# Optimization experiments

Measured on AMD Instinct MI355X. Metric: run time of the kernel, lower is better.

The kernel has to match this reference:

```python
import jax, jax.numpy as jnp
import numpy as np

B, N, L, D_MODEL, H, D_K, D_V = 8, 307, 64, 64, 4, 16, 16


def setup_inputs() -> dict:
    key = jax.random.key(0)
    ks = jax.random.split(key, 10)
    inp = {
        "input_Q": jax.random.normal(ks[0], (B, N, L, D_MODEL), jnp.float32),
        "input_K": jax.random.normal(ks[1], (B, N, L, D_MODEL), jnp.float32),
        "input_V": jax.random.normal(ks[2], (B, N, L, D_MODEL), jnp.float32),
        "attn_mask": jax.random.uniform(ks[3], (B, N, L, 1), jnp.float32),
        "res_att": jax.random.normal(ks[4], (B, N, H, L, L), jnp.float32),
        # Linear weights stored as [in, out] (torch nn.Linear weight transposed)
        "W_Q": jax.random.normal(ks[5], (D_MODEL, H * D_K), jnp.float32) / np.sqrt(D_MODEL),
        "W_K": jax.random.normal(ks[6], (D_MODEL, H * D_K), jnp.float32) / np.sqrt(D_MODEL),
        "W_V": jax.random.normal(ks[7], (D_MODEL, H * D_V), jnp.float32) / np.sqrt(D_MODEL),
        "W_fc": jax.random.normal(ks[8], (H * D_V, D_MODEL), jnp.float32) / np.sqrt(H * D_V),
        # freshly-constructed nn.LayerNorm has weight=1, bias=0
        "ln_scale": jnp.ones((D_MODEL,), jnp.float32),
        "ln_bias": jnp.zeros((D_MODEL,), jnp.float32),
    }
    return inp


def _layernorm(x, scale, bias, eps=1e-5):
    mu = jnp.mean(x, axis=-1, keepdims=True)
    var = jnp.mean(jnp.square(x - mu), axis=-1, keepdims=True)
    return (x - mu) * jax.lax.rsqrt(var + eps) * scale + bias


def reference(input_Q, input_K, input_V, attn_mask, res_att, W_Q, W_K, W_V, W_fc, ln_scale, ln_bias):
    # projections -> [B,N,H,L,d]
    def proj(x, W, d):
        y = jnp.einsum('bnlf,fe->bnle', x, W)
        return y.reshape(B, N, L, H, d).transpose(0, 1, 3, 2, 4)

    Q = proj(input_Q, W_Q, D_K)
    K = proj(input_K, W_K, D_K)
    V = proj(input_V, W_V, D_V)

    # scaled QK^T + residual attention bias: [B,N,H,Lq,Lk]
    scores = jnp.einsum('bnhqd,bnhkd->bnhqk', Q, K) / np.sqrt(D_K) + res_att
    # attn_mask [B,N,L,1] -> broadcast over heads (axis 2) and key dim (last)
    mask = attn_mask[:, :, None, :, :]  # [B,N,1,L,1]
    scores = jnp.where(mask > 0.5, jnp.float32(-1e9), scores)

    # NOTE: original softmaxes over dim=3 (the query axis), faithful here
    attn = jax.nn.softmax(scores, axis=3)
    context = jnp.einsum('bnhqk,bnhkd->bnhqd', attn, V)
    context = context.transpose(0, 1, 3, 2, 4).reshape(B, N, L, H * D_V)
    output = jnp.einsum('bnlc,cf->bnlf', context, W_fc)
    out = _layernorm(output + input_Q, ln_scale, ln_bias)
    return out, scores
```

## Files before the change

### kernel.cpp

```cpp
#include <hip/hip_runtime.h>

#define B_   8
#define N_   307
#define BN   (B_ * N_)
#define OUT_ELEMS (BN * 64 * 64)

typedef float f32x4 __attribute__((ext_vector_type(4)));
typedef short s16x8 __attribute__((ext_vector_type(8)));

__device__ __forceinline__ unsigned short f2bf(float x) {
    unsigned int u = __builtin_bit_cast(unsigned int, x);
    u += 0x7FFFu + ((u >> 16) & 1u);
    return (unsigned short)(u >> 16);
}

__device__ __forceinline__ int swz(int row) { return row ^ ((row >> 3) & 7); }

__device__ __forceinline__ s16x8 ldfrag(const unsigned short* p) {
    return *reinterpret_cast<const s16x8*>(p);
}

__device__ __forceinline__ s16x8 cvt8(float4 lo, float4 hi) {
    s16x8 f;
    f[0] = (short)f2bf(lo.x); f[1] = (short)f2bf(lo.y);
    f[2] = (short)f2bf(lo.z); f[3] = (short)f2bf(lo.w);
    f[4] = (short)f2bf(hi.x); f[5] = (short)f2bf(hi.y);
    f[6] = (short)f2bf(hi.z); f[7] = (short)f2bf(hi.w);
    return f;
}

__device__ __forceinline__ void stage_B(const float* __restrict__ src,
                                        unsigned short* dst, int tid) {
    const float4* s4 = reinterpret_cast<const float4*>(src);
#pragma unroll
    for (int i = 0; i < 4; ++i) {
        int idx = i * 256 + tid;
        float4 v = s4[idx];
        int k  = idx >> 4;
        int n0 = (idx & 15) << 2;
        int ki = k >> 5;
        int qd = (k >> 3) & 3;
        int j  = k & 7;
        float vv[4] = {v.x, v.y, v.z, v.w};
#pragma unroll
        for (int c = 0; c < 4; ++c) {
            int n = n0 + c;
            int row = ((n >> 4) * 2 + ki) * 64 + (qd << 4) + (n & 15);
            dst[(swz(row) << 3) + j] = f2bf(vv[c]);
        }
    }
}

__global__ __launch_bounds__(256, 4) void mta_kernel(
    const float* __restrict__ Xq, const float* __restrict__ Xk,
    const float* __restrict__ Xv, const float* __restrict__ maskp,
    const float* __restrict__ res, const float* __restrict__ Wq,
    const float* __restrict__ Wk, const float* __restrict__ Wv,
    const float* __restrict__ Wfc, const float* __restrict__ lnS,
    const float* __restrict__ lnB, float* __restrict__ out,
    float* __restrict__ scores_out)
{
    __shared__ __align__(16) unsigned char smem[40960];
    unsigned short* sKf = (unsigned short*)(smem);
    unsigned short* sQf = (unsigned short*)(smem + 8192);
    unsigned short* sVf = (unsigned short*)(smem + 16384);
    unsigned short* sW0 = (unsigned short*)(smem + 24576);
    unsigned short* sW1 = (unsigned short*)(smem + 32768);

    const int bn   = blockIdx.x;
    const int tid  = threadIdx.x;
    const int w    = tid >> 6;
    const int lane = tid & 63;
    const int quad = lane >> 4;
    const int l16  = lane & 15;
    const size_t base64 = (size_t)bn * 4096;

    const int soff0 = l16 * 64 + w * 16 + quad * 4;

    bool bmv[4];
#pragma unroll
    for (int nt = 0; nt < 4; ++nt)
        bmv[nt] = maskp[bn * 64 + nt * 16 + l16] > 0.5f;

    f32x4 rA[4];
    {
        const float* rp = res + (((size_t)(bn * 4)) << 12) + soff0;
#pragma unroll
        for (int nt = 0; nt < 4; ++nt)
            rA[nt] = *reinterpret_cast<const f32x4*>(rp + nt * 1024);
    }

#pragma unroll 1
    for (int pj = 0; pj < 3; ++pj) {
        const float* Xs = (pj == 0) ? Xq : (pj == 1) ? Xk : Xv;
        const float* Ws = (pj == 0) ? Wq : (pj == 1) ? Wk : Wv;
        const float* p = Xs + base64 + (w * 16 + l16) * 64 + quad * 8;
        float4 x0 = *(const float4*)(p);      float4 x1 = *(const float4*)(p + 4);
        float4 x2 = *(const float4*)(p + 32); float4 x3 = *(const float4*)(p + 36);
        stage_B(Ws, sW0, tid);
        __syncthreads();
        s16x8 a0 = cvt8(x0, x1);
        s16x8 a1 = cvt8(x2, x3);
#pragma unroll
        for (int nt = 0; nt < 4; ++nt) {
            f32x4 acc = {0.f, 0.f, 0.f, 0.f};
            s16x8 b0 = ldfrag(sW0 + (swz((nt * 2 + 0) * 64 + lane) << 3));
            s16x8 b1 = ldfrag(sW0 + (swz((nt * 2 + 1) * 64 + lane) << 3));
            acc = __builtin_amdgcn_mfma_f32_16x16x32_bf16(a0, b0, acc, 0, 0, 0);
            acc = __builtin_amdgcn_mfma_f32_16x16x32_bf16(a1, b1, acc, 0, 0, 0);
            if (pj == 0) {
#pragma unroll
                for (int r = 0; r < 4; ++r) {
                    int rowq = (nt * 4 + w) * 32 + ((l16 >> 3) << 4) + quad * 4 + r;
                    sQf[(swz(rowq) << 3) + (l16 & 7)] = f2bf(acc[r] * 0.25f);
                }
            } else if (pj == 1) {
#pragma unroll
                for (int r = 0; r < 4; ++r) {
                    int rowk = (nt * 4 + w) * 32 + ((l16 >> 3) << 4) + quad * 4 + r;
                    sKf[(swz(rowk) << 3) + (l16 & 7)] = f2bf(acc[r]);
                }
            } else {
#pragma unroll
                for (int r = 0; r < 4; ++r) {
                    int kk = w * 16 + quad * 4 + r;
                    int rowv = (nt * 2 + (kk >> 5)) * 64 + (((kk >> 3) & 3) << 4) + l16;
                    sVf[(swz(rowv) << 3) + (kk & 7)] = f2bf(acc[r]);
                }
            }
        }
        __syncthreads();
    }

    f32x4 ctx[4];
#pragma unroll
    for (int h = 0; h < 4; ++h) ctx[h] = {0.f, 0.f, 0.f, 0.f};

    const s16x8 zf = {0, 0, 0, 0, 0, 0, 0, 0};
#pragma unroll
    for (int h = 0; h < 4; ++h) {
        const size_t sbase = ((size_t)(bn * 4 + h)) << 12;
        unsigned short* buf = (h & 1) ? sW1 : sW0;

        s16x8 bk = zf;
        if (lane < 32) bk = ldfrag(sKf + (swz((h * 4 + w) * 32 + lane) << 3));

        f32x4 sr[4];
        float esum[4] = {0.f, 0.f, 0.f, 0.f};
#pragma unroll
        for (int nt = 0; nt < 4; ++nt) {
            s16x8 aq = zf;
            if (lane < 32) aq = ldfrag(sQf + (swz((h * 4 + nt) * 32 + lane) << 3));
            f32x4 t = __builtin_amdgcn_mfma_f32_16x16x32_bf16(bk, aq, rA[nt], 0, 0, 0);
#pragma unroll
            for (int r = 0; r < 4; ++r) {
                float s = bmv[nt] ? -1e9f : t[r];
                sr[nt][r] = s;
                esum[r] += __expf(s);
            }
        }
#pragma unroll
        for (int m = 1; m <= 8; m <<= 1)
#pragma unroll
            for (int r = 0; r < 4; ++r)
                esum[r] += __shfl_xor(esum[r], m, 64);
        float inv[4];
#pragma unroll
        for (int r = 0; r < 4; ++r) inv[r] = 1.0f / (esum[r] + 1e-30f);

#pragma unroll
        for (int nt = 0; nt < 4; ++nt) {
            int row = (nt * 2 + (w >> 1)) * 64 + (((w & 1) << 1) + (quad >> 1)) * 16 + l16;
            short4 pk;
            pk.x = (short)f2bf(__expf(sr[nt][0]) * inv[0]);
            pk.y = (short)f2bf(__expf(sr[nt][1]) * inv[1]);
            pk.z = (short)f2bf(__expf(sr[nt][2]) * inv[2]);
            pk.w = (short)f2bf(__expf(sr[nt][3]) * inv[3]);
            *reinterpret_cast<short4*>(buf + (swz(row) << 3) + ((quad & 1) << 2)) = pk;
        }
        __syncthreads();

        if (h < 3) {
            const float* rp2 = res + sbase + 4096 + soff0;
#pragma unroll
            for (int nt = 0; nt < 4; ++nt)
                rA[nt] = *reinterpret_cast<const f32x4*>(rp2 + nt * 1024);
        }
#pragma unroll
        for (int nt = 0; nt < 4; ++nt)
            *reinterpret_cast<f32x4*>(scores_out + sbase + soff0 + nt * 1024) = sr[nt];

#pragma unroll
        for (int ki = 0; ki < 2; ++ki) {
            s16x8 ap = ldfrag(buf + (swz((w * 2 + ki) * 64 + lane) << 3));
            s16x8 bv = ldfrag(sVf + (swz((h * 2 + ki) * 64 + lane) << 3));
            ctx[h] = __builtin_amdgcn_mfma_f32_16x16x32_bf16(ap, bv, ctx[h], 0, 0, 0);
        }
    }
    __syncthreads();

    const int toff = (w * 16 + quad * 4) * 64 + l16;
    float xres[4][4], scl[4], bia[4];
    {
        const float* xp = Xq + base64 + toff;
#pragma unroll
        for (int nt = 0; nt < 4; ++nt) {
#pragma unroll
            for (int r = 0; r < 4; ++r) xres[nt][r] = xp[r * 64 + nt * 16];
            scl[nt] = lnS[nt * 16 + l16];
            bia[nt] = lnB[nt * 16 + l16];
        }
    }
#pragma unroll
    for (int hh = 0; hh < 4; ++hh) {
        int c    = hh * 16 + l16;
        int rowb = (w * 2 + (c >> 5)) * 64 + (((c >> 3) & 3) << 4) + quad * 4;
#pragma unroll
        for (int r = 0; r < 4; ++r)
            sKf[(swz(rowb + r) << 3) + (c & 7)] = f2bf(ctx[hh][r]);
    }
    stage_B(Wfc, sW0, tid);
    __syncthreads();

    f32x4 oacc[4];
    {
        s16x8 a0 = ldfrag(sKf + (swz((w * 2 + 0) * 64 + lane) << 3));
        s16x8 a1 = ldfrag(sKf + (swz((w * 2 + 1) * 64 + lane) << 3));
#pragma unroll
        for (int nt = 0; nt < 4; ++nt) {
            f32x4 a = {0.f, 0.f, 0.f, 0.f};
            s16x8 b0 = ldfrag(sW0 + (swz((nt * 2 + 0) * 64 + lane) << 3));
            s16x8 b1 = ldfrag(sW0 + (swz((nt * 2 + 1) * 64 + lane) << 3));
            a = __builtin_amdgcn_mfma_f32_16x16x32_bf16(a0, b0, a, 0, 0, 0);
            a = __builtin_amdgcn_mfma_f32_16x16x32_bf16(a1, b1, a, 0, 0, 0);
            oacc[nt] = a;
        }
    }

#pragma unroll
    for (int r = 0; r < 4; ++r) {
        float px[4], sum = 0.f, sq = 0.f;
#pragma unroll
        for (int nt = 0; nt < 4; ++nt) {
            float x = oacc[nt][r] + xres[nt][r];
            px[nt] = x; sum += x; sq += x * x;
        }
#pragma unroll
        for (int m = 1; m <= 8; m <<= 1) {
            sum += __shfl_xor(sum, m, 64);
            sq  += __shfl_xor(sq,  m, 64);
        }
        float mu   = sum * 0.015625f;
        float var  = sq * 0.015625f - mu * mu;
        float rstd = rsqrtf(var + 1e-5f);
#pragma unroll
        for (int nt = 0; nt < 4; ++nt) {
            out[base64 + toff + r * 64 + nt * 16] = (px[nt] - mu) * rstd * scl[nt] + bia[nt];
        }
    }
}

extern "C" void kernel_launch(void* const* d_in, const int* in_sizes, int n_in,
                              void* d_out, int out_size, void* d_ws, size_t ws_size,
                              hipStream_t stream) {
    const float* Xq   = (const float*)d_in[0];
    const float* Xk   = (const float*)d_in[1];
    const float* Xv   = (const float*)d_in[2];
    const float* msk  = (const float*)d_in[3];
    const float* res  = (const float*)d_in[4];
    const float* Wq   = (const float*)d_in[5];
    const float* Wk   = (const float*)d_in[6];
    const float* Wv   = (const float*)d_in[7];
    const float* Wfc  = (const float*)d_in[8];
    const float* lnS  = (const float*)d_in[9];
    const float* lnB  = (const float*)d_in[10];
    float* out    = (float*)d_out;
    float* scores = out + OUT_ELEMS;
    mta_kernel<<<BN, 256, 0, stream>>>(Xq, Xk, Xv, msk, res, Wq, Wk, Wv, Wfc,
                                       lnS, lnB, out, scores);
}
```

Measured before the change: 103.1 us.

## Software-pipeline weight and input loads across projection stages with double-buffered LDS

Splits weight staging into a global-load step and an LDS-write step. The projection loop is unrolled so the next projection's weights and inputs are fetched into registers while the current projection's MFMAs run, alternating between two LDS buffers. The Wfc weights, residual input and layernorm parameters are prefetched during the last attention head instead of after it. Softmax exponentials are also kept in registers rather than recomputed. All of this targets global-load latency exposed behind barriers, at the cost of more registers and possible occupancy pressure under launch_bounds(256,4).

```diff
diff --git a/kernel.cpp b/kernel.cpp
--- a/kernel.cpp
+++ b/kernel.cpp
@@ -29,13 +29,19 @@
     return f;
 }
 
-__device__ __forceinline__ void stage_B(const float* __restrict__ src,
-                                        unsigned short* dst, int tid) {
+__device__ __forceinline__ void loadW(const float* __restrict__ src,
+                                      float4 wvv[4], int tid) {
     const float4* s4 = reinterpret_cast<const float4*>(src);
+#pragma unroll
+    for (int i = 0; i < 4; ++i) wvv[i] = s4[i * 256 + tid];
+}
+
+__device__ __forceinline__ void writeW(const float4 wvv[4],
+                                       unsigned short* dst, int tid) {
 #pragma unroll
     for (int i = 0; i < 4; ++i) {
         int idx = i * 256 + tid;
-        float4 v = s4[idx];
+        float4 v = wvv[i];
         int k  = idx >> 4;
         int n0 = (idx & 15) << 2;
         int ki = k >> 5;
@@ -82,6 +88,12 @@
     for (int nt = 0; nt < 4; ++nt)
         bmv[nt] = maskp[bn * 64 + nt * 16 + l16] > 0.5f;
 
+    const int xoff = (w * 16 + l16) * 64 + quad * 8;
+    float4 wv[4];
+    loadW(Wq, wv, tid);
+    const float* pX0 = Xq + base64 + xoff;
+    float4 x00 = *(const float4*)(pX0),      x01 = *(const float4*)(pX0 + 4);
+    float4 x02 = *(const float4*)(pX0 + 32), x03 = *(const float4*)(pX0 + 36);
     f32x4 rA[4];
     {
         const float* rp = res + (((size_t)(bn * 4)) << 12) + soff0;
@@ -89,18 +101,16 @@
         for (int nt = 0; nt < 4; ++nt)
             rA[nt] = *reinterpret_cast<const f32x4*>(rp + nt * 1024);
     }
-
-#pragma unroll 1
-    for (int pj = 0; pj < 3; ++pj) {
-        const float* Xs = (pj == 0) ? Xq : (pj == 1) ? Xk : Xv;
-        const float* Ws = (pj == 0) ? Wq : (pj == 1) ? Wk : Wv;
-        const float* p = Xs + base64 + (w * 16 + l16) * 64 + quad * 8;
-        float4 x0 = *(const float4*)(p);      float4 x1 = *(const float4*)(p + 4);
-        float4 x2 = *(const float4*)(p + 32); float4 x3 = *(const float4*)(p + 36);
-        stage_B(Ws, sW0, tid);
-        __syncthreads();
-        s16x8 a0 = cvt8(x0, x1);
-        s16x8 a1 = cvt8(x2, x3);
+    writeW(wv, sW0, tid);
+    __syncthreads();
+
+    loadW(Wk, wv, tid);
+    const float* pX1 = Xk + base64 + xoff;
+    float4 x10 = *(const float4*)(pX1),      x11 = *(const float4*)(pX1 + 4);
+    float4 x12 = *(const float4*)(pX1 + 32), x13 = *(const float4*)(pX1 + 36);
+    {
+        s16x8 a0 = cvt8(x00, x01);
+        s16x8 a1 = cvt8(x02, x03);
 #pragma unroll
         for (int nt = 0; nt < 4; ++nt) {
             f32x4 acc = {0.f, 0.f, 0.f, 0.f};
@@ -108,33 +118,67 @@
             s16x8 b1 = ldfrag(sW0 + (swz((nt * 2 + 1) * 64 + lane) << 3));
             acc = __builtin_amdgcn_mfma_f32_16x16x32_bf16(a0, b0, acc, 0, 0, 0);
             acc = __builtin_amdgcn_mfma_f32_16x16x32_bf16(a1, b1, acc, 0, 0, 0);
-            if (pj == 0) {
-#pragma unroll
-                for (int r = 0; r < 4; ++r) {
-                    int rowq = (nt * 4 + w) * 32 + ((l16 >> 3) << 4) + quad * 4 + r;
-                    sQf[(swz(rowq) << 3) + (l16 & 7)] = f2bf(acc[r] * 0.25f);
-                }
-            } else if (pj == 1) {
-#pragma unroll
-                for (int r = 0; r < 4; ++r) {
-                    int rowk = (nt * 4 + w) * 32 + ((l16 >> 3) << 4) + quad * 4 + r;
-                    sKf[(swz(rowk) << 3) + (l16 & 7)] = f2bf(acc[r]);
-                }
-            } else {
-#pragma unroll
-                for (int r = 0; r < 4; ++r) {
-                    int kk = w * 16 + quad * 4 + r;
-                    int rowv = (nt * 2 + (kk >> 5)) * 64 + (((kk >> 3) & 3) << 4) + l16;
-                    sVf[(swz(rowv) << 3) + (kk & 7)] = f2bf(acc[r]);
-                }
-            }
-        }
-        __syncthreads();
-    }
+#pragma unroll
+            for (int r = 0; r < 4; ++r) {
+                int rowq = (nt * 4 + w) * 32 + ((l16 >> 3) << 4) + quad * 4 + r;
+                sQf[(swz(rowq) << 3) + (l16 & 7)] = f2bf(acc[r] * 0.25f);
+            }
+        }
+    }
+    writeW(wv, sW1, tid);
+    __syncthreads();
+
+    loadW(Wv, wv, tid);
+    const float* pX2 = Xv + base64 + xoff;
+    float4 x20 = *(const float4*)(pX2),      x21 = *(const float4*)(pX2 + 4);
+    float4 x22 = *(const float4*)(pX2 + 32), x23 = *(const float4*)(pX2 + 36);
+    {
+        s16x8 a0 = cvt8(x10, x11);
+        s16x8 a1 = cvt8(x12, x13);
+#pragma unroll
+        for (int nt = 0; nt < 4; ++nt) {
+            f32x4 acc = {0.f, 0.f, 0.f, 0.f};
+            s16x8 b0 = ldfrag(sW1 + (swz((nt * 2 + 0) * 64 + lane) << 3));
+            s16x8 b1 = ldfrag(sW1 + (swz((nt * 2 + 1) * 64 + lane) << 3));
+            acc = __builtin_amdgcn_mfma_f32_16x16x32_bf16(a0, b0, acc, 0, 0, 0);
+            acc = __builtin_amdgcn_mfma_f32_16x16x32_bf16(a1, b1, acc, 0, 0, 0);
+#pragma unroll
+            for (int r = 0; r < 4; ++r) {
+                int rowk = (nt * 4 + w) * 32 + ((l16 >> 3) << 4) + quad * 4 + r;
+                sKf[(swz(rowk) << 3) + (l16 & 7)] = f2bf(acc[r]);
+            }
+        }
+    }
+    writeW(wv, sW0, tid);
+    __syncthreads();
+
+    {
+        s16x8 a0 = cvt8(x20, x21);
+        s16x8 a1 = cvt8(x22, x23);
+#pragma unroll
+        for (int nt = 0; nt < 4; ++nt) {
+            f32x4 acc = {0.f, 0.f, 0.f, 0.f};
+            s16x8 b0 = ldfrag(sW0 + (swz((nt * 2 + 0) * 64 + lane) << 3));
+            s16x8 b1 = ldfrag(sW0 + (swz((nt * 2 + 1) * 64 + lane) << 3));
+            acc = __builtin_amdgcn_mfma_f32_16x16x32_bf16(a0, b0, acc, 0, 0, 0);
+            acc = __builtin_amdgcn_mfma_f32_16x16x32_bf16(a1, b1, acc, 0, 0, 0);
+#pragma unroll
+            for (int r = 0; r < 4; ++r) {
+                int kk = w * 16 + quad * 4 + r;
+                int rowv = (nt * 2 + (kk >> 5)) * 64 + (((kk >> 3) & 3) << 4) + l16;
+                sVf[(swz(rowv) << 3) + (kk & 7)] = f2bf(acc[r]);
+            }
+        }
+    }
+    __syncthreads();
 
     f32x4 ctx[4];
 #pragma unroll
     for (int h = 0; h < 4; ++h) ctx[h] = {0.f, 0.f, 0.f, 0.f};
+
+    float4 wfc[4];
+    float xres[4][4], scl[4], bia[4];
+    const int toff = (w * 16 + quad * 4) * 64 + l16;
 
     const s16x8 zf = {0, 0, 0, 0, 0, 0, 0, 0};
 #pragma unroll
@@ -146,6 +190,7 @@
         if (lane < 32) bk = ldfrag(sKf + (swz((h * 4 + w) * 32 + lane) << 3));
 
         f32x4 sr[4];
+        float ev[4][4];
         float esum[4] = {0.f, 0.f, 0.f, 0.f};
 #pragma unroll
         for (int nt = 0; nt < 4; ++nt) {
@@ -156,7 +201,9 @@
             for (int r = 0; r < 4; ++r) {
                 float s = bmv[nt] ? -1e9f : t[r];
                 sr[nt][r] = s;
-                esum[r] += __expf(s);
+                float e = __expf(s);
+                ev[nt][r] = e;
+                esum[r] += e;
             }
         }
 #pragma unroll
@@ -172,10 +219,10 @@
         for (int nt = 0; nt < 4; ++nt) {
             int row = (nt * 2 + (w >> 1)) * 64 + (((w & 1) << 1) + (quad >> 1)) * 16 + l16;
             short4 pk;
-            pk.x = (short)f2bf(__expf(sr[nt][0]) * inv[0]);
-            pk.y = (short)f2bf(__expf(sr[nt][1]) * inv[1]);
-            pk.z = (short)f2bf(__expf(sr[nt][2]) * inv[2]);
-            pk.w = (short)f2bf(__expf(sr[nt][3]) * inv[3]);
+            pk.x = (short)f2bf(ev[nt][0] * inv[0]);
+            pk.y = (short)f2bf(ev[nt][1] * inv[1]);
+            pk.z = (short)f2bf(ev[nt][2] * inv[2]);
+            pk.w = (short)f2bf(ev[nt][3] * inv[3]);
             *reinterpret_cast<short4*>(buf + (swz(row) << 3) + ((quad & 1) << 2)) = pk;
         }
         __syncthreads();
@@ -185,6 +232,16 @@
 #pragma unroll
             for (int nt = 0; nt < 4; ++nt)
                 rA[nt] = *reinterpret_cast<const f32x4*>(rp2 + nt * 1024);
+        } else {
+            loadW(Wfc, wfc, tid);
+            const float* xp = Xq + base64 + toff;
+#pragma unroll
+            for (int nt = 0; nt < 4; ++nt) {
+#pragma unroll
+                for (int r = 0; r < 4; ++r) xres[nt][r] = xp[r * 64 + nt * 16];
+                scl[nt] = lnS[nt * 16 + l16];
+                bia[nt] = lnB[nt * 16 + l16];
+            }
         }
 #pragma unroll
         for (int nt = 0; nt < 4; ++nt)
@@ -199,18 +256,6 @@
     }
     __syncthreads();
 
-    const int toff = (w * 16 + quad * 4) * 64 + l16;
-    float xres[4][4], scl[4], bia[4];
-    {
-        const float* xp = Xq + base64 + toff;
-#pragma unroll
-        for (int nt = 0; nt < 4; ++nt) {
-#pragma unroll
-            for (int r = 0; r < 4; ++r) xres[nt][r] = xp[r * 64 + nt * 16];
-            scl[nt] = lnS[nt * 16 + l16];
-            bia[nt] = lnB[nt * 16 + l16];
-        }
-    }
 #pragma unroll
     for (int hh = 0; hh < 4; ++hh) {
         int c    = hh * 16 + l16;
@@ -219,7 +264,7 @@
         for (int r = 0; r < 4; ++r)
             sKf[(swz(rowb + r) << 3) + (c & 7)] = f2bf(ctx[hh][r]);
     }
-    stage_B(Wfc, sW0, tid);
+    writeW(wfc, sW0, tid);
     __syncthreads();
 
     f32x4 oacc[4];
```

Result: no change. 102.7 us (-0.4%).
